# Kernel tuning notes

Hardware: AMD Instinct MI355X
Metric: run time of the kernel (lower is better)

The kernel has to match this reference:

```python
import jax, jax.numpy as jnp
import numpy as np

B, S, H = 2, 2048, 2048
NH, NKV, HD = 32, 8, 64          # num_heads, num_kv_heads, head_dim
G = NH // NKV                     # GQA group size
NEG = -1e9


def setup_inputs() -> dict:
    key = jax.random.key(0)
    ks = jax.random.split(key, 8)
    x = jax.random.normal(ks[0], (B, S, H), dtype=jnp.float32)
    # real RoPE frequencies: theta = 10000 ** (-2i/hd)
    inv_freq = 1.0 / (10000.0 ** (np.arange(0, HD, 2, dtype=np.float32) / HD))
    angles = np.arange(S, dtype=np.float32)[:, None] * inv_freq[None, :]  # [S, HD//2]
    freqs_cos = jnp.asarray(np.cos(angles))
    freqs_sin = jnp.asarray(np.sin(angles))
    # additive causal mask [S, S]
    mask = jnp.where(jnp.tril(jnp.ones((S, S), dtype=bool)), 0.0, NEG).astype(jnp.float32)
    sc = 0.02
    Wq = jax.random.normal(ks[1], (NH * HD, H), dtype=jnp.float32) * sc
    bq = jax.random.normal(ks[2], (NH * HD,), dtype=jnp.float32) * sc
    Wk = jax.random.normal(ks[3], (NKV * HD, H), dtype=jnp.float32) * sc
    bk = jax.random.normal(ks[4], (NKV * HD,), dtype=jnp.float32) * sc
    Wv = jax.random.normal(ks[5], (NKV * HD, H), dtype=jnp.float32) * sc
    bv = jax.random.normal(ks[6], (NKV * HD,), dtype=jnp.float32) * sc
    Wo = jax.random.normal(ks[7], (H, NH * HD), dtype=jnp.float32) * sc
    return {"x": x, "freqs_cos": freqs_cos, "freqs_sin": freqs_sin, "mask": mask,
            "Wq": Wq, "bq": bq, "Wk": Wk, "bk": bk, "Wv": Wv, "bv": bv, "Wo": Wo}


def _rotate_half(t):
    h = t.shape[-1] // 2
    return jnp.concatenate([-t[..., h:], t[..., :h]], axis=-1)


def reference(x, freqs_cos, freqs_sin, mask, Wq, bq, Wk, bk, Wv, bv, Wo):
    b, s, _ = x.shape
    q = (x @ Wq.T + bq).reshape(b, s, NH, HD)
    k = (x @ Wk.T + bk).reshape(b, s, NKV, HD)
    v = (x @ Wv.T + bv).reshape(b, s, NKV, HD)
    # RoPE (rotate_half style): cos/sin duplicated along last dim -> [1, s, 1, HD]
    cos = jnp.concatenate([freqs_cos, freqs_cos], axis=-1)[None, :, None, :]
    sin = jnp.concatenate([freqs_sin, freqs_sin], axis=-1)[None, :, None, :]
    q = q * cos + _rotate_half(q) * sin
    k = k * cos + _rotate_half(k) * sin
    # GQA: view q as [b, s, NKV, G, HD]; avoids repeat_interleave of K/V (same math)
    q5 = q.reshape(b, s, NKV, G, HD)
    scores = jnp.einsum('bqhgd,bkhd->bhgqk', q5, k) / jnp.sqrt(jnp.float32(HD))
    scores = scores + mask  # broadcast [s, s] over [b, h, g, s, s]
    p = jax.nn.softmax(scores.astype(jnp.float32), axis=-1).astype(q.dtype)
    out = jnp.einsum('bhgqk,bkhd->bqhgd', p, v).reshape(b, s, NH * HD)
    return out @ Wo.T
```

## Files before the change

### kernel.cpp

```cpp
#include <hip/hip_runtime.h>
#include <hip/hip_bf16.h>
#include <cstddef>
#include <cstdint>

#define B_   2
#define S_   2048
#define H_   2048
#define NH_  32
#define NKV_ 8
#define HD_  64

typedef __attribute__((ext_vector_type(8))) short short8;
typedef __attribute__((ext_vector_type(4))) float v4f;
typedef __attribute__((ext_vector_type(16))) float v16f;

#define MAXC 48.0f
#define QSCALE 0.18033688011112042f

__device__ __forceinline__ unsigned short f2b(float f) {
    unsigned int u = __float_as_uint(f);
    u += 0x7FFFu + ((u >> 16) & 1u);
    return (unsigned short)(u >> 16);
}
__device__ __forceinline__ unsigned int pkbf(float a, float b) {
    __hip_bfloat162 h = __float22bfloat162_rn(float2{a, b});
    return *(unsigned int*)&h;
}
__device__ __forceinline__ v4f mfma16(short8 a, short8 b, v4f c) {
    return __builtin_amdgcn_mfma_f32_16x16x32_bf16(a, b, c, 0, 0, 0);
}
__device__ __forceinline__ v16f mfma32(short8 a, short8 b, v16f c) {
    return __builtin_amdgcn_mfma_f32_32x32x16_bf16(a, b, c, 0, 0, 0);
}
__device__ __forceinline__ void gll16(void* lds, const void* g) {
    __builtin_amdgcn_global_load_lds(
        (const __attribute__((address_space(1))) unsigned int*)g,
        (__attribute__((address_space(3))) unsigned int*)lds, 16, 0, 0);
}

__global__ __launch_bounds__(256) void convert_all(
    const float* __restrict__ x, const float* __restrict__ wq,
    const float* __restrict__ wk, const float* __restrict__ wv,
    const float* __restrict__ wo,
    unsigned short* __restrict__ xb, unsigned short* __restrict__ wqb,
    unsigned short* __restrict__ wkb, unsigned short* __restrict__ wvb,
    unsigned short* __restrict__ wob)
{
    size_t i = ((size_t)blockIdx.x * 256 + threadIdx.x) * 4;
    const float* src; unsigned short* dst; size_t off;
    if (i < 8388608)       { src = x;  dst = xb;  off = i; }
    else if (i < 12582912) { src = wq; dst = wqb; off = i - 8388608; }
    else if (i < 13631488) { src = wk; dst = wkb; off = i - 12582912; }
    else if (i < 14680064) { src = wv; dst = wvb; off = i - 13631488; }
    else                   { src = wo; dst = wob; off = i - 14680064; }
    float4 v = *(const float4*)(src + off);
    ushort4 o;
    o.x = f2b(v.x); o.y = f2b(v.y); o.z = f2b(v.z); o.w = f2b(v.w);
    *(ushort4*)(dst + off) = o;
}

__global__ __launch_bounds__(256) void qkv_gemm(
    const unsigned short* __restrict__ xb,
    const unsigned short* __restrict__ wqb, const unsigned short* __restrict__ wkb,
    const unsigned short* __restrict__ wvb,
    const float* __restrict__ bq, const float* __restrict__ bk,
    const float* __restrict__ bv,
    const float* __restrict__ fc, const float* __restrict__ fs,
    unsigned short* __restrict__ Qb, unsigned short* __restrict__ Kb,
    unsigned short* __restrict__ Vt)
{
    __shared__ unsigned short As[128 * 64];
    __shared__ unsigned short Bs[128 * 64];
    const int tid = threadIdx.x;
    const int lane = tid & 63, w = tid >> 6;
    const int tx = lane & 15, quad = lane >> 4;
    const int bx = blockIdx.x, by = blockIdx.y;

    const unsigned short *Ap, *Bp;
    int mode, aBase, bBase;
    if (bx < 16)      { mode = 0; Ap = xb;  Bp = wqb; aBase = by * 128; bBase = bx * 128; }
    else if (bx < 20) { mode = 1; Ap = xb;  Bp = wkb; aBase = by * 128; bBase = (bx - 16) * 128; }
    else              { mode = 2; Ap = wvb; Bp = xb;  aBase = (bx - 20) * 128; bBase = by * 128; }

    const int wm = (w >> 1) * 64, wn = (w & 1) * 64;
    v4f acc[4][4];
#pragma unroll
    for (int i = 0; i < 4; ++i)
#pragma unroll
        for (int j = 0; j < 4; ++j) acc[i][j] = (v4f)0.f;

    const int r8 = lane >> 3, gc = (lane & 7) ^ r8;
    const unsigned short* ga = &Ap[(size_t)(aBase + w * 32 + r8) * 2048 + gc * 8];
    const unsigned short* gb = &Bp[(size_t)(bBase + w * 32 + r8) * 2048 + gc * 8];

    const int t7 = tx & 7;
    int slA[2], slB[2];
#pragma unroll
    for (int kk = 0; kk < 2; ++kk) { slA[kk] = ((kk * 4 + quad) ^ t7) * 8; slB[kk] = slA[kk]; }

    for (int k0 = 0; k0 < 2048; k0 += 64) {
        __syncthreads();
#pragma unroll
        for (int i = 0; i < 4; ++i) {
            gll16(&As[(w * 32 + i * 8) * 64], ga + (size_t)(i * 8) * 2048 + k0);
            gll16(&Bs[(w * 32 + i * 8) * 64], gb + (size_t)(i * 8) * 2048 + k0);
        }
        __syncthreads();
#pragma unroll
        for (int kk = 0; kk < 2; ++kk) {
            short8 af[4], bf[4];
#pragma unroll
            for (int mt = 0; mt < 4; ++mt)
                af[mt] = *(const short8*)&As[(wm + mt * 16 + tx) * 64 + slA[kk]];
#pragma unroll
            for (int nt = 0; nt < 4; ++nt)
                bf[nt] = *(const short8*)&Bs[(wn + nt * 16 + tx) * 64 + slB[kk]];
#pragma unroll
            for (int mt = 0; mt < 4; ++mt)
#pragma unroll
                for (int nt = 0; nt < 4; ++nt)
                    acc[mt][nt] = mfma16(af[mt], bf[nt], acc[mt][nt]);
        }
    }

    if (mode <= 1) {
        unsigned short* Cout = mode ? Kb : Qb;
        const float* bias    = mode ? bk : bq;
        const int ldN        = mode ? 512 : 2048;
        const float scq      = mode ? 1.0f : QSCALE;
        float bx0 = bias[bBase + wn +  0 + tx];
        float bx1 = bias[bBase + wn + 16 + tx];
        float bx2 = bias[bBase + wn + 32 + tx];
        float bx3 = bias[bBase + wn + 48 + tx];
#pragma unroll
        for (int mt = 0; mt < 4; ++mt)
#pragma unroll
            for (int rg = 0; rg < 4; ++rg) {
                int m = aBase + wm + mt * 16 + quad * 4 + rg;
                int s = m & (S_ - 1);
                float c0 = fc[s * 32 + tx],      c1 = fc[s * 32 + 16 + tx];
                float s0 = fs[s * 32 + tx],      s1 = fs[s * 32 + 16 + tx];
                float q0 = acc[mt][0][rg] + bx0, q1 = acc[mt][1][rg] + bx1;
                float q2 = acc[mt][2][rg] + bx2, q3 = acc[mt][3][rg] + bx3;
                size_t base = (size_t)m * ldN + bBase + wn + tx;
                Cout[base]      = f2b((q0 * c0 - q2 * s0) * scq);
                Cout[base + 16] = f2b((q1 * c1 - q3 * s1) * scq);
                Cout[base + 32] = f2b((q2 * c0 + q0 * s0) * scq);
                Cout[base + 48] = f2b((q3 * c1 + q1 * s1) * scq);
            }
    } else {
#pragma unroll
        for (int mt = 0; mt < 4; ++mt)
#pragma unroll
            for (int rg = 0; rg < 4; ++rg) {
                int d = aBase + wm + mt * 16 + quad * 4 + rg;
                float bvv = bv[d];
                size_t base = (size_t)d * 4096 + bBase + wn + tx;
#pragma unroll
                for (int nt = 0; nt < 4; ++nt)
                    Vt[base + nt * 16] = f2b(acc[mt][nt][rg] + bvv);
            }
    }
}

__global__ __launch_bounds__(256) void out_gemm(
    const unsigned short* __restrict__ Ab, const unsigned short* __restrict__ Bw,
    float* __restrict__ C)
{
    __shared__ unsigned short As[128 * 64];
    __shared__ unsigned short Bs[128 * 64];
    const int tid = threadIdx.x;
    const int lane = tid & 63, w = tid >> 6;
    const int tx = lane & 15, quad = lane >> 4;
    const int bm = blockIdx.y * 128, bn = blockIdx.x * 128;
    const int wm = (w >> 1) * 64, wn = (w & 1) * 64;

    v4f acc[4][4];
#pragma unroll
    for (int i = 0; i < 4; ++i)
#pragma unroll
        for (int j = 0; j < 4; ++j) acc[i][j] = (v4f)0.f;

    const int r8 = lane >> 3, gc = (lane & 7) ^ r8;
    const unsigned short* ga = &Ab[(size_t)(bm + w * 32 + r8) * 2048 + gc * 8];
    const unsigned short* gb = &Bw[(size_t)(bn + w * 32 + r8) * 2048 + gc * 8];
    const int t7 = tx & 7;
    int sl[2];
#pragma unroll
    for (int kk = 0; kk < 2; ++kk) sl[kk] = ((kk * 4 + quad) ^ t7) * 8;

    for (int k0 = 0; k0 < 2048; k0 += 64) {
        __syncthreads();
#pragma unroll
        for (int i = 0; i < 4; ++i) {
            gll16(&As[(w * 32 + i * 8) * 64], ga + (size_t)(i * 8) * 2048 + k0);
            gll16(&Bs[(w * 32 + i * 8) * 64], gb + (size_t)(i * 8) * 2048 + k0);
        }
        __syncthreads();
#pragma unroll
        for (int kk = 0; kk < 2; ++kk) {
            short8 af[4], bf[4];
#pragma unroll
            for (int mt = 0; mt < 4; ++mt)
                af[mt] = *(const short8*)&As[(wm + mt * 16 + tx) * 64 + sl[kk]];
#pragma unroll
            for (int nt = 0; nt < 4; ++nt)
                bf[nt] = *(const short8*)&Bs[(wn + nt * 16 + tx) * 64 + sl[kk]];
#pragma unroll
            for (int mt = 0; mt < 4; ++mt)
#pragma unroll
                for (int nt = 0; nt < 4; ++nt)
                    acc[mt][nt] = mfma16(af[mt], bf[nt], acc[mt][nt]);
        }
    }
#pragma unroll
    for (int mt = 0; mt < 4; ++mt)
#pragma unroll
        for (int nt = 0; nt < 4; ++nt)
#pragma unroll
            for (int rg = 0; rg < 4; ++rg) {
                int m = bm + wm + mt * 16 + quad * 4 + rg;
                C[(size_t)m * 2048 + bn + wn + nt * 16 + tx] = acc[mt][nt][rg];
            }
}

__global__ __launch_bounds__(256) void attn_mfma(
    const unsigned short* __restrict__ Q, const unsigned short* __restrict__ K,
    const unsigned short* __restrict__ Vt, unsigned short* __restrict__ O)
{
    __shared__ __align__(16) unsigned short Ks[64 * 72];
    __shared__ __align__(16) unsigned short Vs[64 * 72];
    const int tid = threadIdx.x;
    const int lane = tid & 63, wq = tid >> 6;
    const int l32 = lane & 31, half = lane >> 5;
    const int p = blockIdx.x, h = blockIdx.y, b = blockIdx.z;
    const int kvh = h >> 2;
    const int qtw = (wq < 2) ? p : (31 - p);
    const int kt_hi = 31 - p;

    const int qrow = qtw * 64 + (wq & 1) * 32 + l32;
    const unsigned short* Qr = &Q[(((size_t)b * S_ + qrow) * NH_ + h) * HD_];
    short8 qf[4];
#pragma unroll
    for (int s = 0; s < 4; ++s)
        qf[s] = *(const short8*)(Qr + s * 16 + half * 8);

    float l = 0.f;
    v16f o0 = (v16f)0.f, o1 = (v16f)0.f;

    for (int kt = 0; kt <= kt_hi; ++kt) {
        __syncthreads();
#pragma unroll
        for (int i = 0; i < 2; ++i) {
            int e = tid + i * 256;
            int row = e >> 3, c8 = (e & 7) * 8;
            *(uint4*)&Ks[row * 72 + c8] =
                *(const uint4*)&K[(((size_t)b * S_ + kt * 64 + row) * NKV_ + kvh) * HD_ + c8];
            *(uint4*)&Vs[row * 72 + c8] =
                *(const uint4*)&Vt[(size_t)(kvh * 64 + row) * 4096 + b * 2048 + kt * 64 + c8];
        }
        __syncthreads();
        if (kt > qtw) continue;
        const bool diag = (kt == qtw);
        const int tpart = diag ? (wq & 1) : 2;

        for (int t = 0; t < 2; ++t) {
            if (diag && t > tpart) break;
            const int kb = (t * 32 + l32) * 72 + half * 8;
            v16f st = (v16f)(-MAXC);
            st = mfma32(*(const short8*)&Ks[kb],      qf[0], st);
            st = mfma32(*(const short8*)&Ks[kb + 16], qf[1], st);
            st = mfma32(*(const short8*)&Ks[kb + 32], qf[2], st);
            st = mfma32(*(const short8*)&Ks[kb + 48], qf[3], st);
            const bool part = diag && (t == tpart);
            float pv[16];
#pragma unroll
            for (int r = 0; r < 16; ++r) {
                int krow = (r & 3) + 8 * (r >> 2) + 4 * half;
                bool msk = part && (krow > l32);
                pv[r] = msk ? 0.f : exp2f(st[r]);
                l += pv[r];
            }
            unsigned int u[8];
#pragma unroll
            for (int g = 0; g < 4; ++g) {
                u[2 * g]     = pkbf(pv[4 * g],     pv[4 * g + 1]);
                u[2 * g + 1] = pkbf(pv[4 * g + 2], pv[4 * g + 3]);
            }
#pragma unroll
            for (int sg = 0; sg < 2; ++sg) {
                unsigned int a0 = u[4 * sg], a1 = u[4 * sg + 1];
                unsigned int b0 = u[4 * sg + 2], b1 = u[4 * sg + 3];
                unsigned int s0 = __shfl_xor((int)a0, 32);
                unsigned int s1 = __shfl_xor((int)a1, 32);
                unsigned int s2 = __shfl_xor((int)b0, 32);
                unsigned int s3 = __shfl_xor((int)b1, 32);
                uint4 fw;
                fw.x = half ? s2 : a0;
                fw.y = half ? s3 : a1;
                fw.z = half ? b0 : s0;
                fw.w = half ? b1 : s1;
                short8 pf = *(short8*)&fw;
                const int vo = (2 * t + sg) * 16 + half * 8;
                o0 = mfma32(*(const short8*)&Vs[l32 * 72 + vo],        pf, o0);
                o1 = mfma32(*(const short8*)&Vs[(32 + l32) * 72 + vo], pf, o1);
            }
        }
    }

    l += __shfl_xor(l, 32);
    float inv = 1.f / l;
    int qg = qtw * 64 + (wq & 1) * 32 + l32;
    unsigned short* orow = &O[((size_t)b * S_ + qg) * (NH_ * HD_) + h * HD_];
#pragma unroll
    for (int td = 0; td < 2; ++td) {
        const v16f& oo = td ? o1 : o0;
#pragma unroll
        for (int g = 0; g < 4; ++g) {
            int d = td * 32 + g * 8 + half * 4;
            uint2 uu;
            uu.x = pkbf(oo[4 * g] * inv,     oo[4 * g + 1] * inv);
            uu.y = pkbf(oo[4 * g + 2] * inv, oo[4 * g + 3] * inv);
            *(uint2*)&orow[d] = uu;
        }
    }
}

extern "C" void kernel_launch(void* const* d_in, const int* in_sizes, int n_in,
                              void* d_out, int out_size, void* d_ws, size_t ws_size,
                              hipStream_t stream)
{
    const float* x  = (const float*)d_in[0];
    const float* fc = (const float*)d_in[1];
    const float* fs = (const float*)d_in[2];
    const float* Wq = (const float*)d_in[4];
    const float* bq = (const float*)d_in[5];
    const float* Wk = (const float*)d_in[6];
    const float* bk = (const float*)d_in[7];
    const float* Wv = (const float*)d_in[8];
    const float* bv = (const float*)d_in[9];
    const float* Wo = (const float*)d_in[10];
    float* out = (float*)d_out;

    unsigned short* ws = (unsigned short*)d_ws;
    unsigned short* xb  = ws;
    unsigned short* wqb = ws + 8388608;
    unsigned short* wkb = ws + 12582912;
    unsigned short* wvb = ws + 13631488;
    unsigned short* wob = ws + 14680064;
    unsigned short* Qb  = ws + 18874368;
    unsigned short* Kb  = ws + 27262976;
    unsigned short* Vt  = ws + 29360128;
    unsigned short* Ob  = ws + 31457280;

    dim3 blk(256);
    convert_all<<<18432, blk, 0, stream>>>(x, Wq, Wk, Wv, Wo, xb, wqb, wkb, wvb, wob);
    qkv_gemm<<<dim3(24, 32), blk, 0, stream>>>(xb, wqb, wkb, wvb, bq, bk, bv,
                                               fc, fs, Qb, Kb, Vt);
    attn_mfma<<<dim3(16, NH_, B_), blk, 0, stream>>>(Qb, Kb, Vt, Ob);
    out_gemm<<<dim3(16, 32), blk, 0, stream>>>(Ob, wob, out);
}
```

Baseline: 371.5 us.

## Split attention KV range across wave pairs with register-prefetched 128-row tiles

Replaces the paired-query-tile causal balancing with one query tile per block (grid doubled to 32). The two wave pairs split the KV tiles between them, alternating even and odd tiles, and their partial O and l are combined through shared memory at the end. K/V tiles of 128 rows are loaded into registers one iteration ahead, so global loads overlap compute. The trade-offs are an uneven load across blocks, since launch order puts the long rows first, plus a final reduction and more LDS per block.

```diff
diff --git a/kernel.cpp b/kernel.cpp
--- a/kernel.cpp
+++ b/kernel.cpp
@@ -228,45 +228,66 @@
     const unsigned short* __restrict__ Q, const unsigned short* __restrict__ K,
     const unsigned short* __restrict__ Vt, unsigned short* __restrict__ O)
 {
-    __shared__ __align__(16) unsigned short Ks[64 * 72];
-    __shared__ __align__(16) unsigned short Vs[64 * 72];
+    __shared__ __align__(16) unsigned short Ks[128 * 72];
+    __shared__ __align__(16) unsigned short Vs[64 * 136];
     const int tid = threadIdx.x;
     const int lane = tid & 63, wq = tid >> 6;
     const int l32 = lane & 31, half = lane >> 5;
-    const int p = blockIdx.x, h = blockIdx.y, b = blockIdx.z;
+    const int T = 31 - blockIdx.x;
+    const int h = blockIdx.y, b = blockIdx.z;
     const int kvh = h >> 2;
-    const int qtw = (wq < 2) ? p : (31 - p);
-    const int kt_hi = 31 - p;
-
-    const int qrow = qtw * 64 + (wq & 1) * 32 + l32;
+    const int pr = wq >> 1;
+    const int qh = wq & 1;
+    const int L = T + 1;
+    const int niter = (L + 1) >> 1;
+
+    const int qrow = T * 64 + qh * 32 + l32;
     const unsigned short* Qr = &Q[(((size_t)b * S_ + qrow) * NH_ + h) * HD_];
     short8 qf[4];
 #pragma unroll
     for (int s = 0; s < 4; ++s)
         qf[s] = *(const short8*)(Qr + s * 16 + half * 8);
 
+    const unsigned short* gK = K + ((size_t)b * S_) * (NKV_ * HD_) + kvh * HD_
+                               + (size_t)(tid >> 3) * (NKV_ * HD_) + (tid & 7) * 8;
+    const unsigned short* gV = Vt + (size_t)(kvh * 64 + (tid >> 4)) * 4096 + b * 2048
+                               + (tid & 15) * 8;
+    unsigned short* wK = &Ks[(tid >> 3) * 72 + (tid & 7) * 8];
+    unsigned short* wV = &Vs[(tid >> 4) * 136 + (tid & 15) * 8];
+
     float l = 0.f;
     v16f o0 = (v16f)0.f, o1 = (v16f)0.f;
 
-    for (int kt = 0; kt <= kt_hi; ++kt) {
-        __syncthreads();
-#pragma unroll
-        for (int i = 0; i < 2; ++i) {
-            int e = tid + i * 256;
-            int row = e >> 3, c8 = (e & 7) * 8;
-            *(uint4*)&Ks[row * 72 + c8] =
-                *(const uint4*)&K[(((size_t)b * S_ + kt * 64 + row) * NKV_ + kvh) * HD_ + c8];
-            *(uint4*)&Vs[row * 72 + c8] =
-                *(const uint4*)&Vt[(size_t)(kvh * 64 + row) * 4096 + b * 2048 + kt * 64 + c8];
-        }
-        __syncthreads();
-        if (kt > qtw) continue;
-        const bool diag = (kt == qtw);
-        const int tpart = diag ? (wq & 1) : 2;
+    uint4 kr[4], vr[4];
+#pragma unroll
+    for (int i = 0; i < 4; ++i) {
+        kr[i] = *(const uint4*)(gK + (size_t)(i * 32) * (NKV_ * HD_));
+        vr[i] = *(const uint4*)(gV + (size_t)(i * 16) * 4096);
+    }
+
+    for (int it = 0; it < niter; ++it) {
+        __syncthreads();
+#pragma unroll
+        for (int i = 0; i < 4; ++i) {
+            *(uint4*)(wK + i * 32 * 72)  = kr[i];
+            *(uint4*)(wV + i * 16 * 136) = vr[i];
+        }
+        __syncthreads();
+        if (it + 1 < niter) {
+#pragma unroll
+            for (int i = 0; i < 4; ++i) {
+                kr[i] = *(const uint4*)(gK + (size_t)((it + 1) * 128 + i * 32) * (NKV_ * HD_));
+                vr[i] = *(const uint4*)(gV + (it + 1) * 128 + (size_t)(i * 16) * 4096);
+            }
+        }
+        const int kt = 2 * it + pr;
+        if (kt > T) continue;
+        const bool diag = (kt == T);
+        const int tpart = diag ? qh : 2;
 
         for (int t = 0; t < 2; ++t) {
             if (diag && t > tpart) break;
-            const int kb = (t * 32 + l32) * 72 + half * 8;
+            const int kb = (pr * 64 + t * 32 + l32) * 72 + half * 8;
             v16f st = (v16f)(-MAXC);
             st = mfma32(*(const short8*)&Ks[kb],      qf[0], st);
             st = mfma32(*(const short8*)&Ks[kb + 16], qf[1], st);
@@ -301,27 +322,42 @@
                 fw.z = half ? b0 : s0;
                 fw.w = half ? b1 : s1;
                 short8 pf = *(short8*)&fw;
-                const int vo = (2 * t + sg) * 16 + half * 8;
-                o0 = mfma32(*(const short8*)&Vs[l32 * 72 + vo],        pf, o0);
-                o1 = mfma32(*(const short8*)&Vs[(32 + l32) * 72 + vo], pf, o1);
+                const int vo = pr * 64 + (2 * t + sg) * 16 + half * 8;
+                o0 = mfma32(*(const short8*)&Vs[l32 * 136 + vo],        pf, o0);
+                o1 = mfma32(*(const short8*)&Vs[(32 + l32) * 136 + vo], pf, o1);
             }
         }
     }
 
     l += __shfl_xor(l, 32);
-    float inv = 1.f / l;
-    int qg = qtw * 64 + (wq & 1) * 32 + l32;
-    unsigned short* orow = &O[((size_t)b * S_ + qg) * (NH_ * HD_) + h * HD_];
-#pragma unroll
-    for (int td = 0; td < 2; ++td) {
-        const v16f& oo = td ? o1 : o0;
-#pragma unroll
-        for (int g = 0; g < 4; ++g) {
-            int d = td * 32 + g * 8 + half * 4;
-            uint2 uu;
-            uu.x = pkbf(oo[4 * g] * inv,     oo[4 * g + 1] * inv);
-            uu.y = pkbf(oo[4 * g + 2] * inv, oo[4 * g + 3] * inv);
-            *(uint2*)&orow[d] = uu;
+
+    __syncthreads();
+    float* red = (float*)Ks;
+    const int rbase = (qh * 64 + lane) * 33;
+    if (pr == 1) {
+#pragma unroll
+        for (int r = 0; r < 16; ++r) { red[rbase + r] = o0[r]; red[rbase + 16 + r] = o1[r]; }
+        red[rbase + 32] = l;
+    }
+    __syncthreads();
+    if (pr == 0) {
+#pragma unroll
+        for (int r = 0; r < 16; ++r) { o0[r] += red[rbase + r]; o1[r] += red[rbase + 16 + r]; }
+        l += red[rbase + 32];
+        float inv = 1.f / l;
+        int qg = T * 64 + qh * 32 + l32;
+        unsigned short* orow = &O[((size_t)b * S_ + qg) * (NH_ * HD_) + h * HD_];
+#pragma unroll
+        for (int td = 0; td < 2; ++td) {
+            const v16f& oo = td ? o1 : o0;
+#pragma unroll
+            for (int g = 0; g < 4; ++g) {
+                int d = td * 32 + g * 8 + half * 4;
+                uint2 uu;
+                uu.x = pkbf(oo[4 * g] * inv,     oo[4 * g + 1] * inv);
+                uu.y = pkbf(oo[4 * g + 2] * inv, oo[4 * g + 3] * inv);
+                *(uint2*)&orow[d] = uu;
+            }
         }
     }
 }
@@ -357,6 +393,6 @@
     convert_all<<<18432, blk, 0, stream>>>(x, Wq, Wk, Wv, Wo, xb, wqb, wkb, wvb, wob);
     qkv_gemm<<<dim3(24, 32), blk, 0, stream>>>(xb, wqb, wkb, wvb, bq, bk, bv,
                                                fc, fs, Qb, Kb, Vt);
-    attn_mfma<<<dim3(16, NH_, B_), blk, 0, stream>>>(Qb, Kb, Vt, Ob);
+    attn_mfma<<<dim3(32, NH_, B_), blk, 0, stream>>>(Qb, Kb, Vt, Ob);
     out_gemm<<<dim3(16, 32), blk, 0, stream>>>(Ob, wob, out);
 }
```

After: 569.1 us. +53.2%, slower.
